# Kernel tuning notes

Hardware: AMD Instinct MI355X
Metric: run time of the kernel (lower is better)

The kernel has to match this reference:

```python
import jax, jax.numpy as jnp
import numpy as np

TEMPERATURE_F = 0.5
FEATURE_DIM = 1024
CLASS_NUM = 8192


def setup_inputs() -> dict:
    key = jax.random.key(0)
    k1, k2 = jax.random.split(key)
    h_i = jax.random.normal(k1, (FEATURE_DIM, CLASS_NUM), dtype=jnp.float32)
    h_j = jax.random.normal(k2, (FEATURE_DIM, CLASS_NUM), dtype=jnp.float32)
    return {"h_i": h_i, "h_j": h_j}


def reference(h_i, h_j):
    # memory_Loss.forward_modal (NT-Xent over class prototypes)
    C = h_i.shape[1]
    N = 2 * C
    h = jnp.concatenate([h_i, h_j], axis=1)          # [D, N]
    sim = jnp.matmul(h.T, h) / TEMPERATURE_F          # [N, N]
    idx = jnp.arange(N)
    partner = (idx + C) % N                           # positive-pair index per row
    pos = sim[idx, partner]                           # [N] = diag(sim, +C) ++ diag(sim, -C)
    # mask_correlated_samples: drop diagonal and the +/-C partner entry
    mask = (idx[None, :] != idx[:, None]) & (idx[None, :] != partner[:, None])
    neg = jnp.where(mask, sim, -jnp.inf)              # [N, N], N-2 finite per row
    # CrossEntropy(logits=[pos, negs], label=0) = -pos + logsumexp([pos, negs])
    lse = jnp.logaddexp(pos, jax.scipy.special.logsumexp(neg, axis=1))
    loss = jnp.sum(lse - pos) / N
    return loss
```

## Files before the change

### kernel.cpp

```cpp
#include <hip/hip_runtime.h>
#include <stdint.h>

#define FD 1024
#define NC 8192
#define NT 16384
#define NKT 16
#define NTILE2 64
#define NTRI2 2080

typedef __attribute__((ext_vector_type(8))) short bf16x8;
typedef __attribute__((ext_vector_type(4))) float f32x4;

__device__ __forceinline__ unsigned short f2bf(float f) {
  unsigned u = __float_as_uint(f);
  u += 0x7FFF + ((u >> 16) & 1);
  return (unsigned short)(u >> 16);
}
__device__ __forceinline__ float bf2f(unsigned short s) {
  return __uint_as_float(((unsigned)s) << 16);
}

__device__ __forceinline__ void gld16(const void* g, void* l) {
  __builtin_amdgcn_global_load_lds(
      (const __attribute__((address_space(1))) unsigned int*)g,
      (__attribute__((address_space(3))) unsigned int*)l, 16, 0, 0);
}

__device__ __forceinline__ void cas_merge(unsigned long long* p, float m2, float s2) {
  unsigned long long old = *p, assumed;
  do {
    assumed = old;
    float m1 = __uint_as_float((unsigned)(assumed & 0xffffffffull));
    float s1 = __uint_as_float((unsigned)(assumed >> 32));
    float mn = fmaxf(m1, m2);
    float s = s1 * __expf(m1 - mn) + s2 * __expf(m2 - mn);
    unsigned long long nv =
        ((unsigned long long)__float_as_uint(s) << 32) | __float_as_uint(mn);
    old = atomicCAS(p, assumed, nv);
  } while (old != assumed);
}

__global__ void nt_xent_init(unsigned long long* __restrict__ G) {
  G[blockIdx.x * 256 + threadIdx.x] = 0xFF800000ull;
}

__global__ void nt_xent_transpose(const float* __restrict__ hi,
                                  const float* __restrict__ hj,
                                  unsigned short* __restrict__ HT) {
  __shared__ unsigned short tile[64][65];
  const int bn = blockIdx.x, bd = blockIdx.y;
  const int n0 = bn * 64, d0 = bd * 64;
  const float* src = (n0 < NC) ? hi : hj;
  const int nb = (n0 < NC) ? n0 : n0 - NC;
  const int tid = threadIdx.x;
#pragma unroll
  for (int i = 0; i < 16; ++i) {
    int idx = tid + 256 * i;
    int dl = idx >> 6, nl = idx & 63;
    float f = src[(size_t)(d0 + dl) * NC + nb + nl];
    tile[nl][dl] = f2bf(f);
  }
  __syncthreads();
#pragma unroll
  for (int i = 0; i < 16; ++i) {
    int idx = tid + 256 * i;
    int nl = idx >> 6, dl = idx & 63;
    HT[(size_t)(n0 + nl) * FD + d0 + dl] = tile[nl][dl];
  }
}

__global__ __launch_bounds__(512, 2)
void nt_xent_gemm_lse(const unsigned short* __restrict__ HT,
                      unsigned long long* __restrict__ G) {
  __shared__ __align__(16) unsigned char lds[131072];

  const int tid = threadIdx.x;
  const int w = tid >> 6, l = tid & 63;
  const int lr = l & 15;
  const int lk = (l >> 4) * 8;
  const int wr = w >> 2, wc = w & 3;

  int ti, tj;
  {
    const int xcd = blockIdx.x & 7, p = blockIdx.x >> 3;
    if (p < 20) {
      const int hi = (p >= 10) ? 1 : 0;
      const int d = 2 * xcd + hi;
      const int q = p - hi * 10;
      int i = 0;
      while ((i + 1) * 4 - ((i + 1) * i) / 2 <= q) ++i;
      const int j = i + (q - (i * 4 - (i * (i - 1)) / 2));
      ti = d * 4 + i; tj = d * 4 + j;
    } else {
      const int t = p - 20;
      const int o = 15 * xcd + (t >> 4);
      const int q = t & 15;
      int SI = 0;
      while (15 * (SI + 1) - ((SI + 1) * SI) / 2 <= o) ++SI;
      const int SJ = SI + 1 + (o - (15 * SI - (SI * (SI - 1)) / 2));
      ti = SI * 4 + (q >> 2); tj = SJ * 4 + (q & 3);
    }
  }

  const unsigned short* Abase = HT + (((size_t)ti) << 18);
  const unsigned short* Bbase = HT + (((size_t)tj) << 18);

#define STAGE(TT, GRP) do {                                                  \
    const int _t = (TT), _g = (GRP);                                         \
    const int _buf = _t & 1, _kk = (_g >> 1) & 1, _isB = _g & 1;             \
    const unsigned short* _src = _isB ? Bbase : Abase;                       \
    unsigned char* _dst = lds + _buf * 65536 + _isB * 32768 + _kk * 16384;   \
    const int _ko = (_t & 15) * 64 + _kk * 32 + lk;                          \
    const int _mi0 = 2 * w;                                                  \
    gld16(_src + (((size_t)(_mi0 * 16 + lr)) << 10) + _ko,                   \
          _dst + _mi0 * 1024);                                               \
    gld16(_src + (((size_t)((_mi0 + 1) * 16 + lr)) << 10) + _ko,             \
          _dst + (_mi0 + 1) * 1024);                                         \
  } while (0)

#define RDA(BUF, KK, MI) \
  (*(const bf16x8*)(lds + (BUF) * 65536 + (KK) * 16384 + (wr * 8 + (MI)) * 1024 + l * 16))
#define RDB(BUF, KK, N) \
  (*(const bf16x8*)(lds + (BUF) * 65536 + 32768 + (KK) * 16384 + (wc * 4 + (N)) * 1024 + l * 16))

#define MFMA16(MB)                                                           \
  _Pragma("unroll") for (int m = 0; m < 4; ++m)                              \
  _Pragma("unroll") for (int n = 0; n < 4; ++n)                              \
    acc[(MB) + m][n] = __builtin_amdgcn_mfma_f32_16x16x32_bf16(              \
        av[m], bv[n], acc[(MB) + m][n], 0, 0, 0);

  f32x4 acc[8][4];
#pragma unroll
  for (int a = 0; a < 8; ++a)
#pragma unroll
    for (int b = 0; b < 4; ++b) acc[a][b] = (f32x4){0.f, 0.f, 0.f, 0.f};

#pragma unroll
  for (int t0 = 0; t0 < 2; ++t0)
#pragma unroll
    for (int g0 = 0; g0 < 4; ++g0) STAGE(t0, g0);
  asm volatile("s_waitcnt vmcnt(8)" ::: "memory");
  __builtin_amdgcn_s_barrier();

#pragma unroll 2
  for (int T = 0; T < NKT; ++T) {
    const int buf = T & 1;
    bf16x8 av[4], bv[4];

    bv[0] = RDB(buf, 0, 0); bv[1] = RDB(buf, 0, 1);
    bv[2] = RDB(buf, 0, 2); bv[3] = RDB(buf, 0, 3);
    av[0] = RDA(buf, 0, 0); av[1] = RDA(buf, 0, 1);
    av[2] = RDA(buf, 0, 2); av[3] = RDA(buf, 0, 3);
    if (T > 0) STAGE(T + 1, 2);
    __builtin_amdgcn_s_barrier();
    asm volatile("s_waitcnt lgkmcnt(0)" ::: "memory");
    __builtin_amdgcn_s_setprio(1);
    MFMA16(0)
    __builtin_amdgcn_s_setprio(0);
    __builtin_amdgcn_s_barrier();

    av[0] = RDA(buf, 0, 4); av[1] = RDA(buf, 0, 5);
    av[2] = RDA(buf, 0, 6); av[3] = RDA(buf, 0, 7);
    if (T > 0) STAGE(T + 1, 3);
    asm volatile("s_waitcnt vmcnt(8)" ::: "memory");
    __builtin_amdgcn_s_barrier();
    asm volatile("s_waitcnt lgkmcnt(0)" ::: "memory");
    __builtin_amdgcn_s_setprio(1);
    MFMA16(4)
    __builtin_amdgcn_s_setprio(0);
    __builtin_amdgcn_s_barrier();

    bv[0] = RDB(buf, 1, 0); bv[1] = RDB(buf, 1, 1);
    bv[2] = RDB(buf, 1, 2); bv[3] = RDB(buf, 1, 3);
    av[0] = RDA(buf, 1, 0); av[1] = RDA(buf, 1, 1);
    av[2] = RDA(buf, 1, 2); av[3] = RDA(buf, 1, 3);
    STAGE(T + 2, 0);
    __builtin_amdgcn_s_barrier();
    asm volatile("s_waitcnt lgkmcnt(0)" ::: "memory");
    __builtin_amdgcn_s_setprio(1);
    MFMA16(0)
    __builtin_amdgcn_s_setprio(0);
    __builtin_amdgcn_s_barrier();

    av[0] = RDA(buf, 1, 4); av[1] = RDA(buf, 1, 5);
    av[2] = RDA(buf, 1, 6); av[3] = RDA(buf, 1, 7);
    STAGE(T + 2, 1);
    asm volatile("s_waitcnt vmcnt(8)" ::: "memory");
    __builtin_amdgcn_s_barrier();
    asm volatile("s_waitcnt lgkmcnt(0)" ::: "memory");
    __builtin_amdgcn_s_setprio(1);
    MFMA16(4)
    __builtin_amdgcn_s_setprio(0);
    __builtin_amdgcn_s_barrier();
  }

  asm volatile("s_waitcnt vmcnt(0)" ::: "memory");
  __builtin_amdgcn_s_barrier();

  float (*red)[4][128][2] = (float (*)[4][128][2])lds;
  float (*redc)[2][64][2] = (float (*)[2][64][2])(lds + 8192);

  const int gr0 = ti * 256 + wr * 128 + ((l >> 4) << 2);
  const int gc0 = tj * 256 + wc * 64 + lr;

#pragma unroll
  for (int m = 0; m < 8; ++m) {
#pragma unroll
    for (int rg = 0; rg < 4; ++rg) {
      const int grow = gr0 + m * 16 + rg;
      float vs[4];
      float mx = -INFINITY;
#pragma unroll
      for (int n = 0; n < 4; ++n) {
        float v = acc[m][n][rg] * 2.0f;
        if (gc0 + n * 16 == grow) v = -INFINITY;
        vs[n] = v;
        mx = fmaxf(mx, v);
      }
#pragma unroll
      for (int off = 1; off < 16; off <<= 1) mx = fmaxf(mx, __shfl_xor(mx, off, 16));
      float sm = 0.f;
#pragma unroll
      for (int n = 0; n < 4; ++n) sm += __expf(vs[n] - mx);
#pragma unroll
      for (int off = 1; off < 16; off <<= 1) sm += __shfl_xor(sm, off, 16);
      if (lr == 0) {
        const int rl = m * 16 + ((l >> 4) << 2) + rg;
        red[wr][wc][rl][0] = mx;
        red[wr][wc][rl][1] = sm;
      }
    }
  }

  if (ti != tj) {
#pragma unroll
    for (int n = 0; n < 4; ++n) {
      float mx = -INFINITY;
#pragma unroll
      for (int m = 0; m < 8; ++m)
#pragma unroll
        for (int rg = 0; rg < 4; ++rg) mx = fmaxf(mx, acc[m][n][rg] * 2.0f);
      mx = fmaxf(mx, __shfl_xor(mx, 16));
      mx = fmaxf(mx, __shfl_xor(mx, 32));
      float sm = 0.f;
#pragma unroll
      for (int m = 0; m < 8; ++m)
#pragma unroll
        for (int rg = 0; rg < 4; ++rg) sm += __expf(acc[m][n][rg] * 2.0f - mx);
      sm += __shfl_xor(sm, 16);
      sm += __shfl_xor(sm, 32);
      if (l < 16) {
        redc[wc][wr][n * 16 + lr][0] = mx;
        redc[wc][wr][n * 16 + lr][1] = sm;
      }
    }
  }
  __syncthreads();

  if (tid < 256) {
    const int row = tid, wrr = row >> 7, rl = row & 127;
    float M = -INFINITY;
#pragma unroll
    for (int c = 0; c < 4; ++c) M = fmaxf(M, red[wrr][c][rl][0]);
    float S = 0.f;
#pragma unroll
    for (int c = 0; c < 4; ++c) S += red[wrr][c][rl][1] * __expf(red[wrr][c][rl][0] - M);
    cas_merge(&G[ti * 256 + row], M, S);
  } else if (ti != tj) {
    const int col = tid - 256, wcc = col >> 6, cl = col & 63;
    float m0 = redc[wcc][0][cl][0], s0 = redc[wcc][0][cl][1];
    float m1 = redc[wcc][1][cl][0], s1 = redc[wcc][1][cl][1];
    float mn = fmaxf(m0, m1);
    float s = s0 * __expf(m0 - mn) + s1 * __expf(m1 - mn);
    cas_merge(&G[tj * 256 + col], mn, s);
  }

#undef STAGE
#undef RDA
#undef RDB
#undef MFMA16
}

__global__ void nt_xent_final(const unsigned short* __restrict__ HT,
                              const unsigned long long* __restrict__ G,
                              float* __restrict__ out) {
  const int tid = threadIdx.x;
  const int w = tid >> 6, l = tid & 63;
  const int wave = blockIdx.x * 4 + w;
  float local = 0.f;
  for (int rr = 0; rr < 16; ++rr) {
    int i = wave * 16 + rr;
    int p = (i + NC) & (NT - 1);
    const int4* A = (const int4*)(HT + (((size_t)i) << 10) + (l << 4));
    const int4* B = (const int4*)(HT + (((size_t)p) << 10) + (l << 4));
    union { int4 v; unsigned short u[8]; } a0, a1, b0, b1;
    a0.v = A[0]; a1.v = A[1]; b0.v = B[0]; b1.v = B[1];
    float dot = 0.f;
#pragma unroll
    for (int j = 0; j < 8; ++j) dot += bf2f(a0.u[j]) * bf2f(b0.u[j]);
#pragma unroll
    for (int j = 0; j < 8; ++j) dot += bf2f(a1.u[j]) * bf2f(b1.u[j]);
#pragma unroll
    for (int off = 1; off < 64; off <<= 1) dot += __shfl_xor(dot, off, 64);
    if (l == 0) {
      unsigned long long g = G[i];
      float m = __uint_as_float((unsigned)(g & 0xffffffffull));
      float s = __uint_as_float((unsigned)(g >> 32));
      local += m + __logf(s) - 2.0f * dot;
    }
  }
  if (l == 0) atomicAdd(out, local * (1.0f / (float)NT));
}

extern "C" void kernel_launch(void* const* d_in, const int* in_sizes, int n_in,
                              void* d_out, int out_size, void* d_ws, size_t ws_size,
                              hipStream_t stream) {
  const float* hi = (const float*)d_in[0];
  const float* hj = (const float*)d_in[1];
  unsigned short* HT = (unsigned short*)d_ws;
  unsigned long long* G = (unsigned long long*)((char*)d_ws + (size_t)NT * FD * 2);
  float* out = (float*)d_out;

  const size_t need = (size_t)NT * FD * 2 + (size_t)NT * 8;
  if (ws_size < need) return;

  hipMemsetAsync(out, 0, sizeof(float), stream);
  nt_xent_init<<<NT / 256, 256, 0, stream>>>(G);
  nt_xent_transpose<<<dim3(NT / 64, FD / 64), 256, 0, stream>>>(hi, hj, HT);
  nt_xent_gemm_lse<<<NTRI2, 512, 0, stream>>>(HT, G);
  nt_xent_final<<<NT / 64, 256, 0, stream>>>(HT, G, out);
}
```

Measured before the change: 547.0 us.

## Make GEMM-LSE kernel persistent with cross-tile prefetch of next tile's first k-slice

Replaces the 2080-block grid with 256 persistent blocks, one per CU, each looping over its tiles (stride 32 in slot index). The last k-step of the current tile prefetches the first k-slice of the next tile, so global loads overlap the LSE epilogue and tile transitions. The reduction scratch moves to a separate LDS region so the epilogue does not clobber the staged data. Occupancy drops to one 512-thread block per CU, which limits latency hiding from a second resident block.

```diff
diff --git a/kernel.cpp b/kernel.cpp
--- a/kernel.cpp
+++ b/kernel.cpp
@@ -5,7 +5,6 @@
 #define NC 8192
 #define NT 16384
 #define NKT 16
-#define NTILE2 64
 #define NTRI2 2080
 
 typedef __attribute__((ext_vector_type(8))) short bf16x8;
@@ -40,6 +39,26 @@
   } while (old != assumed);
 }
 
+__device__ __forceinline__ void decode_tile(int xcd, int p, int& ti, int& tj) {
+  if (p < 20) {
+    const int hi = (p >= 10) ? 1 : 0;
+    const int d = 2 * xcd + hi;
+    const int q = p - hi * 10;
+    int i = 0;
+    while ((i + 1) * 4 - ((i + 1) * i) / 2 <= q) ++i;
+    const int j = i + (q - (i * 4 - (i * (i - 1)) / 2));
+    ti = d * 4 + i; tj = d * 4 + j;
+  } else {
+    const int t = p - 20;
+    const int o = 15 * xcd + (t >> 4);
+    const int q = t & 15;
+    int SI = 0;
+    while (15 * (SI + 1) - ((SI + 1) * SI) / 2 <= o) ++SI;
+    const int SJ = SI + 1 + (o - (15 * SI - (SI * (SI - 1)) / 2));
+    ti = SI * 4 + (q >> 2); tj = SJ * 4 + (q & 3);
+  }
+}
+
 __global__ void nt_xent_init(unsigned long long* __restrict__ G) {
   G[blockIdx.x * 256 + threadIdx.x] = 0xFF800000ull;
 }
@@ -69,10 +88,10 @@
   }
 }
 
-__global__ __launch_bounds__(512, 2)
+__global__ __launch_bounds__(512, 1)
 void nt_xent_gemm_lse(const unsigned short* __restrict__ HT,
                       unsigned long long* __restrict__ G) {
-  __shared__ __align__(16) unsigned char lds[131072];
+  __shared__ __align__(16) unsigned char lds[143360];
 
   const int tid = threadIdx.x;
   const int w = tid >> 6, l = tid & 63;
@@ -80,42 +99,16 @@
   const int lk = (l >> 4) * 8;
   const int wr = w >> 2, wc = w & 3;
 
-  int ti, tj;
-  {
-    const int xcd = blockIdx.x & 7, p = blockIdx.x >> 3;
-    if (p < 20) {
-      const int hi = (p >= 10) ? 1 : 0;
-      const int d = 2 * xcd + hi;
-      const int q = p - hi * 10;
-      int i = 0;
-      while ((i + 1) * 4 - ((i + 1) * i) / 2 <= q) ++i;
-      const int j = i + (q - (i * 4 - (i * (i - 1)) / 2));
-      ti = d * 4 + i; tj = d * 4 + j;
-    } else {
-      const int t = p - 20;
-      const int o = 15 * xcd + (t >> 4);
-      const int q = t & 15;
-      int SI = 0;
-      while (15 * (SI + 1) - ((SI + 1) * SI) / 2 <= o) ++SI;
-      const int SJ = SI + 1 + (o - (15 * SI - (SI * (SI - 1)) / 2));
-      ti = SI * 4 + (q >> 2); tj = SJ * 4 + (q & 3);
-    }
-  }
-
-  const unsigned short* Abase = HT + (((size_t)ti) << 18);
-  const unsigned short* Bbase = HT + (((size_t)tj) << 18);
-
-#define STAGE(TT, GRP) do {                                                  \
-    const int _t = (TT), _g = (GRP);                                         \
-    const int _buf = _t & 1, _kk = (_g >> 1) & 1, _isB = _g & 1;             \
-    const unsigned short* _src = _isB ? Bbase : Abase;                       \
-    unsigned char* _dst = lds + _buf * 65536 + _isB * 32768 + _kk * 16384;   \
-    const int _ko = (_t & 15) * 64 + _kk * 32 + lk;                          \
-    const int _mi0 = 2 * w;                                                  \
-    gld16(_src + (((size_t)(_mi0 * 16 + lr)) << 10) + _ko,                   \
-          _dst + _mi0 * 1024);                                               \
-    gld16(_src + (((size_t)((_mi0 + 1) * 16 + lr)) << 10) + _ko,             \
-          _dst + (_mi0 + 1) * 1024);                                         \
+  const int xcd = blockIdx.x & 7;
+  const int slot = blockIdx.x >> 3;
+
+#define STAGE2(AB, BB, KO, DBUF, KK, ISB) do {                               \
+    const unsigned short* _s = (ISB) ? (BB) : (AB);                          \
+    unsigned char* _d = lds + (DBUF) * 65536 + (ISB) * 32768 +               \
+                        (KK) * 16384 + (2 * w) * 1024;                       \
+    const int _ko = (KO) + (KK) * 32 + lk;                                   \
+    gld16(_s + (((size_t)(2 * w * 16 + lr)) << 10) + _ko, _d);               \
+    gld16(_s + (((size_t)((2 * w + 1) * 16 + lr)) << 10) + _ko, _d + 1024);  \
   } while (0)
 
 #define RDA(BUF, KK, MI) \
@@ -129,156 +122,173 @@
     acc[(MB) + m][n] = __builtin_amdgcn_mfma_f32_16x16x32_bf16(              \
         av[m], bv[n], acc[(MB) + m][n], 0, 0, 0);
 
+#define VM4 asm volatile("s_waitcnt vmcnt(4)" ::: "memory")
+#define BARW do { __builtin_amdgcn_s_barrier();                              \
+    asm volatile("s_waitcnt lgkmcnt(0)" ::: "memory");                       \
+    __builtin_amdgcn_sched_barrier(0); } while (0)
+
+#define KTILE(BUF, NA, NB, NKO) do {                                         \
+    bv[0] = RDB(BUF, 0, 0); bv[1] = RDB(BUF, 0, 1);                          \
+    bv[2] = RDB(BUF, 0, 2); bv[3] = RDB(BUF, 0, 3);                          \
+    av[0] = RDA(BUF, 0, 0); av[1] = RDA(BUF, 0, 1);                          \
+    av[2] = RDA(BUF, 0, 2); av[3] = RDA(BUF, 0, 3);                          \
+    STAGE2(NA, NB, NKO, (BUF) ^ 1, 0, 0);                                    \
+    BARW;                                                                    \
+    __builtin_amdgcn_s_setprio(1); MFMA16(0) __builtin_amdgcn_s_setprio(0);  \
+    __builtin_amdgcn_s_barrier();                                            \
+    av[0] = RDA(BUF, 0, 4); av[1] = RDA(BUF, 0, 5);                          \
+    av[2] = RDA(BUF, 0, 6); av[3] = RDA(BUF, 0, 7);                          \
+    STAGE2(NA, NB, NKO, (BUF) ^ 1, 0, 1);                                    \
+    VM4;                                                                     \
+    BARW;                                                                    \
+    __builtin_amdgcn_s_setprio(1); MFMA16(4) __builtin_amdgcn_s_setprio(0);  \
+    __builtin_amdgcn_s_barrier();                                            \
+    bv[0] = RDB(BUF, 1, 0); bv[1] = RDB(BUF, 1, 1);                          \
+    bv[2] = RDB(BUF, 1, 2); bv[3] = RDB(BUF, 1, 3);                          \
+    av[0] = RDA(BUF, 1, 0); av[1] = RDA(BUF, 1, 1);                          \
+    av[2] = RDA(BUF, 1, 2); av[3] = RDA(BUF, 1, 3);                          \
+    STAGE2(NA, NB, NKO, (BUF) ^ 1, 1, 0);                                    \
+    BARW;                                                                    \
+    __builtin_amdgcn_s_setprio(1); MFMA16(0) __builtin_amdgcn_s_setprio(0);  \
+    __builtin_amdgcn_s_barrier();                                            \
+    av[0] = RDA(BUF, 1, 4); av[1] = RDA(BUF, 1, 5);                          \
+    av[2] = RDA(BUF, 1, 6); av[3] = RDA(BUF, 1, 7);                          \
+    STAGE2(NA, NB, NKO, (BUF) ^ 1, 1, 1);                                    \
+    VM4;                                                                     \
+    BARW;                                                                    \
+    __builtin_amdgcn_s_setprio(1); MFMA16(4) __builtin_amdgcn_s_setprio(0);  \
+    __builtin_amdgcn_s_barrier();                                            \
+  } while (0)
+
   f32x4 acc[8][4];
 #pragma unroll
   for (int a = 0; a < 8; ++a)
 #pragma unroll
     for (int b = 0; b < 4; ++b) acc[a][b] = (f32x4){0.f, 0.f, 0.f, 0.f};
-
-#pragma unroll
-  for (int t0 = 0; t0 < 2; ++t0)
-#pragma unroll
-    for (int g0 = 0; g0 < 4; ++g0) STAGE(t0, g0);
-  asm volatile("s_waitcnt vmcnt(8)" ::: "memory");
-  __builtin_amdgcn_s_barrier();
-
-#pragma unroll 2
-  for (int T = 0; T < NKT; ++T) {
-    const int buf = T & 1;
-    bf16x8 av[4], bv[4];
-
-    bv[0] = RDB(buf, 0, 0); bv[1] = RDB(buf, 0, 1);
-    bv[2] = RDB(buf, 0, 2); bv[3] = RDB(buf, 0, 3);
-    av[0] = RDA(buf, 0, 0); av[1] = RDA(buf, 0, 1);
-    av[2] = RDA(buf, 0, 2); av[3] = RDA(buf, 0, 3);
-    if (T > 0) STAGE(T + 1, 2);
-    __builtin_amdgcn_s_barrier();
-    asm volatile("s_waitcnt lgkmcnt(0)" ::: "memory");
-    __builtin_amdgcn_s_setprio(1);
-    MFMA16(0)
-    __builtin_amdgcn_s_setprio(0);
-    __builtin_amdgcn_s_barrier();
-
-    av[0] = RDA(buf, 0, 4); av[1] = RDA(buf, 0, 5);
-    av[2] = RDA(buf, 0, 6); av[3] = RDA(buf, 0, 7);
-    if (T > 0) STAGE(T + 1, 3);
-    asm volatile("s_waitcnt vmcnt(8)" ::: "memory");
-    __builtin_amdgcn_s_barrier();
-    asm volatile("s_waitcnt lgkmcnt(0)" ::: "memory");
-    __builtin_amdgcn_s_setprio(1);
-    MFMA16(4)
-    __builtin_amdgcn_s_setprio(0);
-    __builtin_amdgcn_s_barrier();
-
-    bv[0] = RDB(buf, 1, 0); bv[1] = RDB(buf, 1, 1);
-    bv[2] = RDB(buf, 1, 2); bv[3] = RDB(buf, 1, 3);
-    av[0] = RDA(buf, 1, 0); av[1] = RDA(buf, 1, 1);
-    av[2] = RDA(buf, 1, 2); av[3] = RDA(buf, 1, 3);
-    STAGE(T + 2, 0);
-    __builtin_amdgcn_s_barrier();
-    asm volatile("s_waitcnt lgkmcnt(0)" ::: "memory");
-    __builtin_amdgcn_s_setprio(1);
-    MFMA16(0)
-    __builtin_amdgcn_s_setprio(0);
-    __builtin_amdgcn_s_barrier();
-
-    av[0] = RDA(buf, 1, 4); av[1] = RDA(buf, 1, 5);
-    av[2] = RDA(buf, 1, 6); av[3] = RDA(buf, 1, 7);
-    STAGE(T + 2, 1);
-    asm volatile("s_waitcnt vmcnt(8)" ::: "memory");
-    __builtin_amdgcn_s_barrier();
-    asm volatile("s_waitcnt lgkmcnt(0)" ::: "memory");
-    __builtin_amdgcn_s_setprio(1);
-    MFMA16(4)
-    __builtin_amdgcn_s_setprio(0);
-    __builtin_amdgcn_s_barrier();
-  }
-
+  bf16x8 av[4], bv[4];
+
+  int p = slot, ti, tj;
+  decode_tile(xcd, p, ti, tj);
+  const unsigned short* Acur = HT + (((size_t)ti) << 18);
+  const unsigned short* Bcur = HT + (((size_t)tj) << 18);
+  STAGE2(Acur, Bcur, 0, 0, 0, 0);
+  STAGE2(Acur, Bcur, 0, 0, 0, 1);
+  STAGE2(Acur, Bcur, 0, 0, 1, 0);
+  STAGE2(Acur, Bcur, 0, 0, 1, 1);
   asm volatile("s_waitcnt vmcnt(0)" ::: "memory");
   __builtin_amdgcn_s_barrier();
 
-  float (*red)[4][128][2] = (float (*)[4][128][2])lds;
-  float (*redc)[2][64][2] = (float (*)[2][64][2])(lds + 8192);
-
-  const int gr0 = ti * 256 + wr * 128 + ((l >> 4) << 2);
-  const int gc0 = tj * 256 + wc * 64 + lr;
-
-#pragma unroll
-  for (int m = 0; m < 8; ++m) {
-#pragma unroll
-    for (int rg = 0; rg < 4; ++rg) {
-      const int grow = gr0 + m * 16 + rg;
-      float vs[4];
-      float mx = -INFINITY;
-#pragma unroll
-      for (int n = 0; n < 4; ++n) {
-        float v = acc[m][n][rg] * 2.0f;
-        if (gc0 + n * 16 == grow) v = -INFINITY;
-        vs[n] = v;
-        mx = fmaxf(mx, v);
+  while (true) {
+    const int pn = p + 32;
+    const bool has_next = (pn < 260);
+    int tin = 0, tjn = 0;
+    if (has_next) decode_tile(xcd, pn, tin, tjn);
+    const unsigned short* Anx = HT + (((size_t)tin) << 18);
+    const unsigned short* Bnx = HT + (((size_t)tjn) << 18);
+
+#pragma unroll 1
+    for (int Tp = 0; Tp < 7; ++Tp) {
+      KTILE(0, Acur, Bcur, (2 * Tp + 1) * 64);
+      KTILE(1, Acur, Bcur, (2 * Tp + 2) * 64);
+    }
+    KTILE(0, Acur, Bcur, 15 * 64);
+    KTILE(1, Anx, Bnx, 0);
+
+    {
+      float (*red)[4][128][2] = (float (*)[4][128][2])(lds + 131072);
+      float (*redc)[2][64][2] = (float (*)[2][64][2])(lds + 139264);
+      const int gr0 = ti * 256 + wr * 128 + ((l >> 4) << 2);
+      const int gc0 = tj * 256 + wc * 64 + lr;
+#pragma unroll
+      for (int m = 0; m < 8; ++m) {
+#pragma unroll
+        for (int rg = 0; rg < 4; ++rg) {
+          const int grow = gr0 + m * 16 + rg;
+          float vs[4];
+          float mx = -INFINITY;
+#pragma unroll
+          for (int n = 0; n < 4; ++n) {
+            float v = acc[m][n][rg] * 2.0f;
+            if (gc0 + n * 16 == grow) v = -INFINITY;
+            vs[n] = v;
+            mx = fmaxf(mx, v);
+          }
+#pragma unroll
+          for (int off = 1; off < 16; off <<= 1) mx = fmaxf(mx, __shfl_xor(mx, off, 16));
+          float sm = 0.f;
+#pragma unroll
+          for (int n = 0; n < 4; ++n) sm += __expf(vs[n] - mx);
+#pragma unroll
+          for (int off = 1; off < 16; off <<= 1) sm += __shfl_xor(sm, off, 16);
+          if (lr == 0) {
+            const int rl = m * 16 + ((l >> 4) << 2) + rg;
+            red[wr][wc][rl][0] = mx;
+            red[wr][wc][rl][1] = sm;
+          }
+        }
       }
-#pragma unroll
-      for (int off = 1; off < 16; off <<= 1) mx = fmaxf(mx, __shfl_xor(mx, off, 16));
-      float sm = 0.f;
-#pragma unroll
-      for (int n = 0; n < 4; ++n) sm += __expf(vs[n] - mx);
-#pragma unroll
-      for (int off = 1; off < 16; off <<= 1) sm += __shfl_xor(sm, off, 16);
-      if (lr == 0) {
-        const int rl = m * 16 + ((l >> 4) << 2) + rg;
-        red[wr][wc][rl][0] = mx;
-        red[wr][wc][rl][1] = sm;
+      if (ti != tj) {
+#pragma unroll
+        for (int n = 0; n < 4; ++n) {
+          float mx = -INFINITY;
+#pragma unroll
+          for (int m = 0; m < 8; ++m)
+#pragma unroll
+            for (int rg = 0; rg < 4; ++rg) mx = fmaxf(mx, acc[m][n][rg] * 2.0f);
+          mx = fmaxf(mx, __shfl_xor(mx, 16));
+          mx = fmaxf(mx, __shfl_xor(mx, 32));
+          float sm = 0.f;
+#pragma unroll
+          for (int m = 0; m < 8; ++m)
+#pragma unroll
+            for (int rg = 0; rg < 4; ++rg) sm += __expf(acc[m][n][rg] * 2.0f - mx);
+          sm += __shfl_xor(sm, 16);
+          sm += __shfl_xor(sm, 32);
+          if (l < 16) {
+            redc[wc][wr][n * 16 + lr][0] = mx;
+            redc[wc][wr][n * 16 + lr][1] = sm;
+          }
+        }
       }
+#pragma unroll
+      for (int a = 0; a < 8; ++a)
+#pragma unroll
+        for (int b = 0; b < 4; ++b) acc[a][b] = (f32x4){0.f, 0.f, 0.f, 0.f};
+
+      asm volatile("s_waitcnt lgkmcnt(0)" ::: "memory");
+      __builtin_amdgcn_s_barrier();
+
+      if (tid < 256) {
+        const int row = tid, wrr = row >> 7, rl = row & 127;
+        float M = -INFINITY;
+#pragma unroll
+        for (int c = 0; c < 4; ++c) M = fmaxf(M, red[wrr][c][rl][0]);
+        float S = 0.f;
+#pragma unroll
+        for (int c = 0; c < 4; ++c) S += red[wrr][c][rl][1] * __expf(red[wrr][c][rl][0] - M);
+        cas_merge(&G[ti * 256 + row], M, S);
+      } else if (ti != tj) {
+        const int col = tid - 256, wcc = col >> 6, cl = col & 63;
+        float m0 = redc[wcc][0][cl][0], s0 = redc[wcc][0][cl][1];
+        float m1 = redc[wcc][1][cl][0], s1 = redc[wcc][1][cl][1];
+        float mn = fmaxf(m0, m1);
+        float s = s0 * __expf(m0 - mn) + s1 * __expf(m1 - mn);
+        cas_merge(&G[tj * 256 + col], mn, s);
+      }
+      __builtin_amdgcn_s_barrier();
     }
-  }
-
-  if (ti != tj) {
-#pragma unroll
-    for (int n = 0; n < 4; ++n) {
-      float mx = -INFINITY;
-#pragma unroll
-      for (int m = 0; m < 8; ++m)
-#pragma unroll
-        for (int rg = 0; rg < 4; ++rg) mx = fmaxf(mx, acc[m][n][rg] * 2.0f);
-      mx = fmaxf(mx, __shfl_xor(mx, 16));
-      mx = fmaxf(mx, __shfl_xor(mx, 32));
-      float sm = 0.f;
-#pragma unroll
-      for (int m = 0; m < 8; ++m)
-#pragma unroll
-        for (int rg = 0; rg < 4; ++rg) sm += __expf(acc[m][n][rg] * 2.0f - mx);
-      sm += __shfl_xor(sm, 16);
-      sm += __shfl_xor(sm, 32);
-      if (l < 16) {
-        redc[wc][wr][n * 16 + lr][0] = mx;
-        redc[wc][wr][n * 16 + lr][1] = sm;
-      }
-    }
-  }
-  __syncthreads();
-
-  if (tid < 256) {
-    const int row = tid, wrr = row >> 7, rl = row & 127;
-    float M = -INFINITY;
-#pragma unroll
-    for (int c = 0; c < 4; ++c) M = fmaxf(M, red[wrr][c][rl][0]);
-    float S = 0.f;
-#pragma unroll
-    for (int c = 0; c < 4; ++c) S += red[wrr][c][rl][1] * __expf(red[wrr][c][rl][0] - M);
-    cas_merge(&G[ti * 256 + row], M, S);
-  } else if (ti != tj) {
-    const int col = tid - 256, wcc = col >> 6, cl = col & 63;
-    float m0 = redc[wcc][0][cl][0], s0 = redc[wcc][0][cl][1];
-    float m1 = redc[wcc][1][cl][0], s1 = redc[wcc][1][cl][1];
-    float mn = fmaxf(m0, m1);
-    float s = s0 * __expf(m0 - mn) + s1 * __expf(m1 - mn);
-    cas_merge(&G[tj * 256 + col], mn, s);
-  }
-
-#undef STAGE
+
+    if (!has_next) break;
+    p = pn; ti = tin; tj = tjn; Acur = Anx; Bcur = Bnx;
+  }
+
+#undef STAGE2
 #undef RDA
 #undef RDB
 #undef MFMA16
+#undef VM4
+#undef BARW
+#undef KTILE
 }
 
 __global__ void nt_xent_final(const unsigned short* __restrict__ HT,
@@ -327,6 +337,6 @@
   hipMemsetAsync(out, 0, sizeof(float), stream);
   nt_xent_init<<<NT / 256, 256, 0, stream>>>(G);
   nt_xent_transpose<<<dim3(NT / 64, FD / 64), 256, 0, stream>>>(hi, hj, HT);
-  nt_xent_gemm_lse<<<NTRI2, 512, 0, stream>>>(HT, G);
+  nt_xent_gemm_lse<<<256, 512, 0, stream>>>(HT, G);
   nt_xent_final<<<NT / 64, 256, 0, stream>>>(HT, G, out);
 }
```

Result: faster. 524.0 us (-4.2%).
